# Kernel tuning notes

Hardware: AMD Instinct MI355X
Metric: run time of the kernel (lower is better)

Reference implementation:

```python
import jax, jax.numpy as jnp
import numpy as np

BS, V, C, A = 8, 4096, 64, 12   # batch, vertices, channels, anchors (anchor_size=12 hardcoded in source)
K = 4                            # neighbor_num
POOLING_RATE = 4
POOL = V // POOLING_RATE


def setup_inputs() -> dict:
    key = jax.random.key(0)
    k1, k2, k3 = jax.random.split(key, 3)
    vertices = jax.random.normal(k1, (BS, V, 3), dtype=jnp.float32)
    feature_map = jax.random.normal(k2, (BS, C, V, A), dtype=jnp.float32)
    # deterministic stand-in for torch.randperm(V)[:POOL]
    sample_idx = jax.random.permutation(k3, V)[:POOL].astype(jnp.int32)
    return {"vertices": vertices, "feature_map": feature_map, "sample_idx": sample_idx}


def reference(vertices, feature_map, sample_idx):
    bs, v, _ = vertices.shape
    c, a = feature_map.shape[1], feature_map.shape[3]
    k = K
    # pairwise squared euclidean distances: (bs, v, v)
    inner = jnp.einsum('bic,bjc->bij', vertices, vertices)
    quad = jnp.sum(vertices * vertices, axis=2)                     # (bs, v)
    dist = -2.0 * inner + quad[:, None, :] + quad[:, :, None]
    # k+1 smallest, drop self (first entry)
    _, idx = jax.lax.top_k(-dist, k + 1)                            # (bs, v, k+1)
    nbr = idx[:, :, 1:]                                             # (bs, v, k)
    # gather neighbor features along vertex axis (axis=2 of feature_map)
    idx_b = jnp.broadcast_to(nbr.reshape(bs, 1, v * k, 1), (bs, c, v * k, a))
    nbr_feat = jnp.take_along_axis(feature_map, idx_b, axis=2)      # (bs, c, v*k, a)
    nbr_feat = nbr_feat.reshape(bs, c, v, k, a)
    pooled = jnp.max(nbr_feat, axis=3)                              # (bs, c, v, a)
    vertices_pool = vertices[:, sample_idx, :]                      # (bs, pool, 3)
    feature_map_pool = pooled[:, :, sample_idx, :]                  # (bs, c, pool, a)
    return vertices_pool, feature_map_pool
```

## Files before the change

### kernel.cpp

```cpp
#include <hip/hip_runtime.h>
#include <stdint.h>

#define BS 8
#define V 4096
#define C 64
#define A 12
#define POOL 1024

template<int NCC>
__global__ __launch_bounds__(256) void knn_chunk_kernel(
    const float* __restrict__ vtx,
    const int* __restrict__ sidx,
    unsigned long long* __restrict__ partial)
{
    constexpr int CC = V / NCC;
    __shared__ float4 cand[CC];

    const int bid = blockIdx.x;
    const int cc = bid % NCC;
    const int qc = (bid / NCC) & 3;
    const int b  = bid / (NCC * 4);
    const int tid = threadIdx.x;

    const float* vb = vtx + (size_t)b * V * 3;

    for (int t = tid; t < CC; t += 256) {
        const int j = cc * CC + t;
        const float x = vb[j * 3 + 0];
        const float y = vb[j * 3 + 1];
        const float z = vb[j * 3 + 2];
        float q;
        {
#pragma clang fp contract(off)
            q = (x * x + y * y) + z * z;
        }
        cand[t] = make_float4(x, y, z, q);
    }
    __syncthreads();

    const int s = qc * 256 + tid;
    const int gq = sidx[s];
    const float qx = vb[gq * 3 + 0];
    const float qy = vb[gq * 3 + 1];
    const float qz = vb[gq * 3 + 2];
    float qq;
    {
#pragma clang fp contract(off)
        qq = (qx * qx + qy * qy) + qz * qz;
    }

    unsigned int h0 = ~0u, h1 = ~0u, h2 = ~0u, h3 = ~0u, h4 = ~0u;
    unsigned int l0 = 0, l1 = 0, l2 = 0, l3 = 0, l4 = 0;

#pragma unroll 8
    for (int jj = 0; jj < CC; ++jj) {
        const float4 cd = cand[jj];
        const float inner = fmaf(cd.z, qz, fmaf(cd.y, qy, cd.x * qx));
        const float d = fmaf(-2.0f, inner, cd.w) + qq;
        const unsigned int bits = __float_as_uint(d);
        const unsigned int u = bits ^ ((unsigned int)(((int)bits) >> 31) | 0x80000000u);
        const unsigned int idx = (unsigned int)(cc * CC + jj);
        if (u < h4) {
            const bool c0 = u < h0, c1 = u < h1, c2 = u < h2, c3 = u < h3;
            h4 = c3 ? h3 : u;              l4 = c3 ? l3 : idx;
            h3 = c3 ? (c2 ? h2 : u) : h3;  l3 = c3 ? (c2 ? l2 : idx) : l3;
            h2 = c2 ? (c1 ? h1 : u) : h2;  l2 = c2 ? (c1 ? l1 : idx) : l2;
            h1 = c1 ? (c0 ? h0 : u) : h1;  l1 = c1 ? (c0 ? l0 : idx) : l1;
            h0 = c0 ? u : h0;              l0 = c0 ? idx : l0;
        }
    }

    unsigned long long* p = partial + ((size_t)(b * POOL + s) * NCC + cc) * 5;
    p[0] = ((unsigned long long)h0 << 32) | l0;
    p[1] = ((unsigned long long)h1 << 32) | l1;
    p[2] = ((unsigned long long)h2 << 32) | l2;
    p[3] = ((unsigned long long)h3 << 32) | l3;
    p[4] = ((unsigned long long)h4 << 32) | l4;
}

template<int NCC>
__global__ __launch_bounds__(256) void knn_merge_kernel(
    const unsigned long long* __restrict__ partial,
    const float* __restrict__ vtx,
    const int* __restrict__ sidx,
    int* __restrict__ nbr,
    float* __restrict__ outv)
{
    const int t = blockIdx.x * 256 + threadIdx.x;
    const int b = t / POOL;
    const int s = t % POOL;

    const unsigned long long* p = partial + (size_t)t * (NCC * 5);

    unsigned int h0 = ~0u, h1 = ~0u, h2 = ~0u, h3 = ~0u, h4 = ~0u;
    unsigned int l0 = 0, l1 = 0, l2 = 0, l3 = 0, l4 = 0;

#pragma unroll 4
    for (int ccc = 0; ccc < NCC; ++ccc) {
        const unsigned long long a0 = p[ccc * 5 + 0];
        const unsigned long long a1 = p[ccc * 5 + 1];
        const unsigned long long a2 = p[ccc * 5 + 2];
        const unsigned long long a3 = p[ccc * 5 + 3];
        const unsigned long long a4 = p[ccc * 5 + 4];
        if ((unsigned int)(a0 >> 32) < h4) {
#define INS(K)                                                               \
            {                                                                \
                const unsigned int u = (unsigned int)((K) >> 32);            \
                const unsigned int idx = (unsigned int)(K);                  \
                const bool c0 = u < h0, c1 = u < h1, c2 = u < h2,            \
                           c3 = u < h3, c4 = u < h4;                         \
                h4 = c4 ? (c3 ? h3 : u) : h4;                                \
                l4 = c4 ? (c3 ? l3 : idx) : l4;                              \
                h3 = c3 ? (c2 ? h2 : u) : h3;                                \
                l3 = c3 ? (c2 ? l2 : idx) : l3;                              \
                h2 = c2 ? (c1 ? h1 : u) : h2;                                \
                l2 = c2 ? (c1 ? l1 : idx) : l2;                              \
                h1 = c1 ? (c0 ? h0 : u) : h1;                                \
                l1 = c1 ? (c0 ? l0 : idx) : l1;                              \
                h0 = c0 ? u : h0;                                            \
                l0 = c0 ? idx : l0;                                          \
            }
            INS(a0) INS(a1) INS(a2) INS(a3) INS(a4)
#undef INS
        }
    }

    int4 nb;
    nb.x = (int)l1;
    nb.y = (int)l2;
    nb.z = (int)l3;
    nb.w = (int)l4;
    ((int4*)nbr)[t] = nb;

    const int gq = sidx[s];
    const float* vv = vtx + ((size_t)b * V + gq) * 3;
    outv[(size_t)t * 3 + 0] = vv[0];
    outv[(size_t)t * 3 + 1] = vv[1];
    outv[(size_t)t * 3 + 2] = vv[2];
}

__device__ inline float4 f4max(float4 a, float4 b) {
    return make_float4(fmaxf(a.x, b.x), fmaxf(a.y, b.y),
                       fmaxf(a.z, b.z), fmaxf(a.w, b.w));
}

__global__ __launch_bounds__(256) void gather_pool_kernel(
    const float* __restrict__ fm,
    const int* __restrict__ nbr,
    float* __restrict__ outf)
{
    const int t = blockIdx.x * 256 + threadIdx.x;
    const int s = t % POOL;
    const int c = (t / POOL) % C;
    const int b = t / (POOL * C);

    const int4 nb = ((const int4*)nbr)[b * POOL + s];

    const float4* base = (const float4*)fm + (size_t)(b * C + c) * V * 3;

    float4 r0 = base[(size_t)nb.x * 3 + 0];
    float4 r1 = base[(size_t)nb.x * 3 + 1];
    float4 r2 = base[(size_t)nb.x * 3 + 2];

    float4 s0 = base[(size_t)nb.y * 3 + 0];
    float4 s1 = base[(size_t)nb.y * 3 + 1];
    float4 s2 = base[(size_t)nb.y * 3 + 2];
    r0 = f4max(r0, s0); r1 = f4max(r1, s1); r2 = f4max(r2, s2);

    s0 = base[(size_t)nb.z * 3 + 0];
    s1 = base[(size_t)nb.z * 3 + 1];
    s2 = base[(size_t)nb.z * 3 + 2];
    r0 = f4max(r0, s0); r1 = f4max(r1, s1); r2 = f4max(r2, s2);

    s0 = base[(size_t)nb.w * 3 + 0];
    s1 = base[(size_t)nb.w * 3 + 1];
    s2 = base[(size_t)nb.w * 3 + 2];
    r0 = f4max(r0, s0); r1 = f4max(r1, s1); r2 = f4max(r2, s2);

    float4* dst = (float4*)outf + (size_t)t * 3;
    dst[0] = r0;
    dst[1] = r1;
    dst[2] = r2;
}

extern "C" void kernel_launch(void* const* d_in, const int* in_sizes, int n_in,
                              void* d_out, int out_size, void* d_ws, size_t ws_size,
                              hipStream_t stream) {
    const float* vtx = (const float*)d_in[0];
    const float* fm  = (const float*)d_in[1];
    const int* sidx  = (const int*)d_in[2];
    float* out = (float*)d_out;

    float* outv = out;
    float* outf = out + (size_t)BS * POOL * 3;

    unsigned long long* partial = (unsigned long long*)d_ws;

    const size_t need32 = (size_t)BS * POOL * 32 * 5 * 8 + (size_t)BS * POOL * 16;

    if (ws_size >= need32) {
        constexpr int NCC = 32;
        int* nbr = (int*)((char*)d_ws + (size_t)BS * POOL * NCC * 5 * 8);
        knn_chunk_kernel<NCC><<<BS * 4 * NCC, 256, 0, stream>>>(vtx, sidx, partial);
        knn_merge_kernel<NCC><<<(BS * POOL) / 256, 256, 0, stream>>>(partial, vtx, sidx, nbr, outv);
        gather_pool_kernel<<<(BS * C * POOL) / 256, 256, 0, stream>>>(fm, nbr, outf);
    } else {
        constexpr int NCC = 16;
        int* nbr = (int*)((char*)d_ws + (size_t)BS * POOL * NCC * 5 * 8);
        knn_chunk_kernel<NCC><<<BS * 4 * NCC, 256, 0, stream>>>(vtx, sidx, partial);
        knn_merge_kernel<NCC><<<(BS * POOL) / 256, 256, 0, stream>>>(partial, vtx, sidx, nbr, outv);
        gather_pool_kernel<<<(BS * C * POOL) / 256, 256, 0, stream>>>(fm, nbr, outf);
    }
}
```

Measured before the change: 225.7 us.

## Invert neighbor gather into CSR scatter with shared-memory atomic max pooling

```diff
diff --git a/kernel.cpp b/kernel.cpp
--- a/kernel.cpp
+++ b/kernel.cpp
@@ -7,20 +7,32 @@
 #define A 12
 #define POOL 1024
 
+__device__ inline unsigned int ordu(float f) {
+    unsigned int b = __float_as_uint(f);
+    return b ^ ((unsigned int)(((int)b) >> 31) | 0x80000000u);
+}
+__device__ inline float unordu(unsigned int u) {
+    unsigned int m = (~((unsigned int)(((int)u) >> 31))) | 0x80000000u;
+    return __uint_as_float(u ^ m);
+}
+
 template<int NCC>
 __global__ __launch_bounds__(256) void knn_chunk_kernel(
     const float* __restrict__ vtx,
     const int* __restrict__ sidx,
-    unsigned long long* __restrict__ partial)
+    unsigned long long* __restrict__ partial,
+    unsigned int* __restrict__ counts)
 {
     constexpr int CC = V / NCC;
     __shared__ float4 cand[CC];
 
     const int bid = blockIdx.x;
+    const int tid = threadIdx.x;
+    if (bid < (BS * V) / 256) counts[bid * 256 + tid] = 0;
+
     const int cc = bid % NCC;
     const int qc = (bid / NCC) & 3;
     const int b  = bid / (NCC * 4);
-    const int tid = threadIdx.x;
 
     const float* vb = vtx + (size_t)b * V * 3;
 
@@ -84,7 +96,8 @@
     const float* __restrict__ vtx,
     const int* __restrict__ sidx,
     int* __restrict__ nbr,
-    float* __restrict__ outv)
+    float* __restrict__ outv,
+    unsigned int* __restrict__ counts)
 {
     const int t = blockIdx.x * 256 + threadIdx.x;
     const int b = t / POOL;
@@ -132,6 +145,12 @@
     nb.w = (int)l4;
     ((int4*)nbr)[t] = nb;
 
+    unsigned int* cb = counts + b * V;
+    atomicAdd(&cb[l1], 1u);
+    atomicAdd(&cb[l2], 1u);
+    atomicAdd(&cb[l3], 1u);
+    atomicAdd(&cb[l4], 1u);
+
     const int gq = sidx[s];
     const float* vv = vtx + ((size_t)b * V + gq) * 3;
     outv[(size_t)t * 3 + 0] = vv[0];
@@ -139,48 +158,115 @@
     outv[(size_t)t * 3 + 2] = vv[2];
 }
 
-__device__ inline float4 f4max(float4 a, float4 b) {
-    return make_float4(fmaxf(a.x, b.x), fmaxf(a.y, b.y),
-                       fmaxf(a.z, b.z), fmaxf(a.w, b.w));
-}
-
-__global__ __launch_bounds__(256) void gather_pool_kernel(
+__global__ __launch_bounds__(256) void scan_kernel(
+    const unsigned int* __restrict__ counts,
+    unsigned int* __restrict__ rowptr,
+    unsigned int* __restrict__ cursors)
+{
+    const int b = blockIdx.x;
+    const int tid = threadIdx.x;
+    __shared__ unsigned int psum[256];
+
+    const unsigned int* cb = counts + b * V;
+    unsigned int local[16];
+    unsigned int sum = 0;
+#pragma unroll
+    for (int i = 0; i < 16; ++i) { local[i] = sum; sum += cb[tid * 16 + i]; }
+    psum[tid] = sum;
+    __syncthreads();
+
+    for (int off = 1; off < 256; off <<= 1) {
+        unsigned int v = (tid >= off) ? psum[tid - off] : 0u;
+        __syncthreads();
+        psum[tid] += v;
+        __syncthreads();
+    }
+    const unsigned int base = (tid == 0) ? 0u : psum[tid - 1];
+
+    unsigned int* rp = rowptr + b * (V + 1);
+    unsigned int* cu = cursors + b * V;
+#pragma unroll
+    for (int i = 0; i < 16; ++i) {
+        const unsigned int e = base + local[i];
+        rp[tid * 16 + i] = e;
+        cu[tid * 16 + i] = e;
+    }
+    if (tid == 255) rp[V] = base + sum;
+}
+
+__global__ __launch_bounds__(256) void fill_kernel(
+    const int* __restrict__ nbr,
+    unsigned int* __restrict__ cursors,
+    unsigned int* __restrict__ entries)
+{
+    const int t = blockIdx.x * 256 + threadIdx.x;
+    const int b = t / POOL;
+    const unsigned int s = (unsigned int)(t % POOL);
+    const int4 nb = ((const int4*)nbr)[t];
+    unsigned int* cu = cursors + b * V;
+    unsigned int* en = entries + b * 4096;
+    en[atomicAdd(&cu[nb.x], 1u)] = s;
+    en[atomicAdd(&cu[nb.y], 1u)] = s;
+    en[atomicAdd(&cu[nb.z], 1u)] = s;
+    en[atomicAdd(&cu[nb.w], 1u)] = s;
+}
+
+__global__ __launch_bounds__(512) void pool_kernel(
     const float* __restrict__ fm,
-    const int* __restrict__ nbr,
+    const unsigned int* __restrict__ rowptr,
+    const unsigned int* __restrict__ entries,
     float* __restrict__ outf)
 {
-    const int t = blockIdx.x * 256 + threadIdx.x;
-    const int s = t % POOL;
-    const int c = (t / POOL) % C;
-    const int b = t / (POOL * C);
-
-    const int4 nb = ((const int4*)nbr)[b * POOL + s];
-
-    const float4* base = (const float4*)fm + (size_t)(b * C + c) * V * 3;
-
-    float4 r0 = base[(size_t)nb.x * 3 + 0];
-    float4 r1 = base[(size_t)nb.x * 3 + 1];
-    float4 r2 = base[(size_t)nb.x * 3 + 2];
-
-    float4 s0 = base[(size_t)nb.y * 3 + 0];
-    float4 s1 = base[(size_t)nb.y * 3 + 1];
-    float4 s2 = base[(size_t)nb.y * 3 + 2];
-    r0 = f4max(r0, s0); r1 = f4max(r1, s1); r2 = f4max(r2, s2);
-
-    s0 = base[(size_t)nb.z * 3 + 0];
-    s1 = base[(size_t)nb.z * 3 + 1];
-    s2 = base[(size_t)nb.z * 3 + 2];
-    r0 = f4max(r0, s0); r1 = f4max(r1, s1); r2 = f4max(r2, s2);
-
-    s0 = base[(size_t)nb.w * 3 + 0];
-    s1 = base[(size_t)nb.w * 3 + 1];
-    s2 = base[(size_t)nb.w * 3 + 2];
-    r0 = f4max(r0, s0); r1 = f4max(r1, s1); r2 = f4max(r2, s2);
-
-    float4* dst = (float4*)outf + (size_t)t * 3;
-    dst[0] = r0;
-    dst[1] = r1;
-    dst[2] = r2;
+    __shared__ unsigned int pl[POOL * A];
+    const int c = blockIdx.x % C;
+    const int b = blockIdx.x / C;
+    const int tid = threadIdx.x;
+
+    {
+        uint4* p4 = (uint4*)pl;
+        const uint4 z = make_uint4(0u, 0u, 0u, 0u);
+#pragma unroll
+        for (int i = 0; i < 6; ++i) p4[tid + i * 512] = z;
+    }
+    __syncthreads();
+
+    const unsigned int* rp = rowptr + b * (V + 1);
+    const unsigned int* en = entries + b * 4096;
+    const float4* plane = (const float4*)(fm + (size_t)(b * C + c) * V * A);
+
+#pragma unroll 1
+    for (int it = 0; it < V / 512; ++it) {
+        const int j = it * 512 + tid;
+        const unsigned int beg = rp[j];
+        const unsigned int end = rp[j + 1];
+        if (beg == end) continue;
+
+        const float4 f0 = plane[j * 3 + 0];
+        const float4 f1 = plane[j * 3 + 1];
+        const float4 f2 = plane[j * 3 + 2];
+        const unsigned int u0 = ordu(f0.x), u1 = ordu(f0.y), u2  = ordu(f0.z), u3  = ordu(f0.w);
+        const unsigned int u4 = ordu(f1.x), u5 = ordu(f1.y), u6  = ordu(f1.z), u7  = ordu(f1.w);
+        const unsigned int u8 = ordu(f2.x), u9 = ordu(f2.y), u10 = ordu(f2.z), u11 = ordu(f2.w);
+
+        for (unsigned int e = beg; e < end; ++e) {
+            unsigned int* d = pl + en[e] * A;
+            atomicMax(d + 0, u0);  atomicMax(d + 1, u1);  atomicMax(d + 2, u2);
+            atomicMax(d + 3, u3);  atomicMax(d + 4, u4);  atomicMax(d + 5, u5);
+            atomicMax(d + 6, u6);  atomicMax(d + 7, u7);  atomicMax(d + 8, u8);
+            atomicMax(d + 9, u9);  atomicMax(d + 10, u10); atomicMax(d + 11, u11);
+        }
+    }
+    __syncthreads();
+
+    const uint4* p4 = (const uint4*)pl;
+    float4* dst = (float4*)(outf + (size_t)(b * C + c) * POOL * A);
+#pragma unroll
+    for (int i = 0; i < 6; ++i) {
+        const uint4 v = p4[tid + i * 512];
+        float4 f;
+        f.x = unordu(v.x); f.y = unordu(v.y); f.z = unordu(v.z); f.w = unordu(v.w);
+        dst[tid + i * 512] = f;
+    }
 }
 
 extern "C" void kernel_launch(void* const* d_in, const int* in_sizes, int n_in,
@@ -194,21 +280,36 @@
     float* outv = out;
     float* outf = out + (size_t)BS * POOL * 3;
 
-    unsigned long long* partial = (unsigned long long*)d_ws;
-
-    const size_t need32 = (size_t)BS * POOL * 32 * 5 * 8 + (size_t)BS * POOL * 16;
-
-    if (ws_size >= need32) {
+    char* ws = (char*)d_ws;
+    const size_t partial32_b = (size_t)BS * POOL * 32 * 5 * 8;
+    const size_t partial16_b = (size_t)BS * POOL * 16 * 5 * 8;
+    const size_t nbr_b     = (size_t)BS * POOL * 4 * 4;
+    const size_t counts_b  = (size_t)BS * V * 4;
+    const size_t rowptr_b  = (size_t)BS * (V + 1) * 4 + 28;
+    const size_t cursors_b = (size_t)BS * V * 4;
+    const size_t entries_b = (size_t)BS * 4096 * 4;
+    const size_t tail_b = nbr_b + counts_b + rowptr_b + cursors_b + entries_b;
+
+    const bool big = ws_size >= partial32_b + tail_b;
+    const size_t partial_b = big ? partial32_b : partial16_b;
+
+    unsigned long long* partial = (unsigned long long*)ws;
+    int* nbr            = (int*)(ws + partial_b);
+    unsigned int* counts  = (unsigned int*)(ws + partial_b + nbr_b);
+    unsigned int* rowptr  = (unsigned int*)(ws + partial_b + nbr_b + counts_b);
+    unsigned int* cursors = (unsigned int*)(ws + partial_b + nbr_b + counts_b + rowptr_b);
+    unsigned int* entries = (unsigned int*)(ws + partial_b + nbr_b + counts_b + rowptr_b + cursors_b);
+
+    if (big) {
         constexpr int NCC = 32;
-        int* nbr = (int*)((char*)d_ws + (size_t)BS * POOL * NCC * 5 * 8);
-        knn_chunk_kernel<NCC><<<BS * 4 * NCC, 256, 0, stream>>>(vtx, sidx, partial);
-        knn_merge_kernel<NCC><<<(BS * POOL) / 256, 256, 0, stream>>>(partial, vtx, sidx, nbr, outv);
-        gather_pool_kernel<<<(BS * C * POOL) / 256, 256, 0, stream>>>(fm, nbr, outf);
+        knn_chunk_kernel<NCC><<<BS * 4 * NCC, 256, 0, stream>>>(vtx, sidx, partial, counts);
+        knn_merge_kernel<NCC><<<(BS * POOL) / 256, 256, 0, stream>>>(partial, vtx, sidx, nbr, outv, counts);
     } else {
         constexpr int NCC = 16;
-        int* nbr = (int*)((char*)d_ws + (size_t)BS * POOL * NCC * 5 * 8);
-        knn_chunk_kernel<NCC><<<BS * 4 * NCC, 256, 0, stream>>>(vtx, sidx, partial);
-        knn_merge_kernel<NCC><<<(BS * POOL) / 256, 256, 0, stream>>>(partial, vtx, sidx, nbr, outv);
-        gather_pool_kernel<<<(BS * C * POOL) / 256, 256, 0, stream>>>(fm, nbr, outf);
-    }
-}
+        knn_chunk_kernel<NCC><<<BS * 4 * NCC, 256, 0, stream>>>(vtx, sidx, partial, counts);
+        knn_merge_kernel<NCC><<<(BS * POOL) / 256, 256, 0, stream>>>(partial, vtx, sidx, nbr, outv, counts);
+    }
+    scan_kernel<<<BS, 256, 0, stream>>>(counts, rowptr, cursors);
+    fill_kernel<<<(BS * POOL) / 256, 256, 0, stream>>>(nbr, cursors, entries);
+    pool_kernel<<<BS * C, 512, 0, stream>>>(fm, rowptr, entries, outf);
+}
```

Result: no change. 229.1 us (+1.5%).
